# Optimization experiments

Hardware: AMD Instinct MI355X
Metric: run time of the kernel (lower is better)

The kernel has to match this reference:

```python
import jax, jax.numpy as jnp
import numpy as np

B, T, C = 2, 2048, 2048
H, KVH = 16, 4
HD = C // H            # head_dim = 128
REP = H // KVH         # q heads per kv head = 4


def _alibi_slopes(n_head):
    # get_slopes_power_of_2: start = 2^(-2^-(log2(H)-3)); s_h = start * start^h
    start = 2.0 ** (-(2.0 ** (-(np.log2(n_head) - 3.0))))
    return jnp.asarray([start ** (i + 1) for i in range(n_head)], jnp.float32)


def setup_inputs() -> dict:
    key = jax.random.key(0)
    ks = jax.random.split(key, 4)
    sc = 0.02
    return {
        "x": jax.random.normal(ks[0], (B, T, C), jnp.float32),
        "Wq": jax.random.normal(ks[1], (C, C), jnp.float32) * sc,
        "Wkv": jax.random.normal(ks[2], (C, HD * KVH * 2), jnp.float32) * sc,
        "Wo": jax.random.normal(ks[3], (C, C), jnp.float32) * sc,
        "bo": jnp.zeros((C,), jnp.float32),
    }


def reference(x, Wq, Wkv, Wo, bo):
    Bv, Tv, Cv = x.shape
    # projections
    q = (x @ Wq).reshape(Bv, Tv, H, HD).transpose(0, 2, 1, 3)      # (B,H,T,hd)
    k, v = jnp.split(x @ Wkv, 2, axis=-1)
    k = k.reshape(Bv, Tv, KVH, HD).transpose(0, 2, 1, 3)           # (B,KVH,T,hd)
    v = v.reshape(Bv, Tv, KVH, HD).transpose(0, 2, 1, 3)
    # torch .repeat tiles kv heads: query head h = r*KVH + g uses kv head g.
    qg = q.reshape(Bv, REP, KVH, Tv, HD)
    scores = jnp.einsum('brgtd,bgsd->brgts', qg, k) / jnp.sqrt(jnp.float32(HD))
    # ALiBi bias: tril((j - i) * slope_h), zero on/above diagonal region handled by causal mask
    idx = jnp.arange(Tv)
    diff = (idx[None, :] - idx[:, None]).astype(jnp.float32)       # j - i (negative below diag)
    slopes = _alibi_slopes(H).reshape(REP, KVH)                    # head h = r*KVH+g
    bias = jnp.tril(diff)[None, None] * slopes[:, :, None, None]   # (REP,KVH,T,T)
    causal = idx[None, :] <= idx[:, None]                          # (T,T)
    scores = jnp.where(causal[None, None, None], scores + bias[None], -jnp.inf)
    attn = jax.nn.softmax(scores, axis=-1)
    out = jnp.einsum('brgts,bgsd->brgtd', attn, v)                 # (B,REP,KVH,T,hd)
    out = out.reshape(Bv, H, Tv, HD).transpose(0, 2, 1, 3).reshape(Bv, Tv, Cv)
    return out @ Wo + bo
```

## Files before the change

kernel.cpp:

```cpp
#include <hip/hip_runtime.h>

typedef __attribute__((ext_vector_type(8))) __bf16 bf16x8;
typedef __attribute__((ext_vector_type(4))) float f32x4;

#define NEG_BIG (-1e30f)

__device__ __forceinline__ unsigned short f2b(float f) {
    unsigned int u = __float_as_uint(f);
    u += 0x7FFFu + ((u >> 16) & 1u);
    return (unsigned short)(u >> 16);
}
__device__ __forceinline__ unsigned cvtpk(float lo, float hi) {
    unsigned r;
    asm("v_cvt_pk_bf16_f32 %0, %1, %2" : "=v"(r) : "v"(lo), "v"(hi));
    return r;
}

typedef const __attribute__((address_space(1))) unsigned int* gas_ptr;
typedef __attribute__((address_space(3))) unsigned int* las_ptr;
__device__ __forceinline__ void gload16(const void* g, void* l) {
    __builtin_amdgcn_global_load_lds((gas_ptr)g, (las_ptr)l, 16, 0, 0);
}

__global__ __launch_bounds__(256) void k_convert(
    const float* __restrict__ x, unsigned short* __restrict__ xb, int n4)
{
    int i = blockIdx.x * 256 + threadIdx.x;
    if (i >= n4) return;
    float4 v = reinterpret_cast<const float4*>(x)[i];
    ushort4 h;
    h.x = f2b(v.x); h.y = f2b(v.y); h.z = f2b(v.z); h.w = f2b(v.w);
    reinterpret_cast<ushort4*>(xb)[i] = h;
}

__global__ __launch_bounds__(256) void k_transpose_all(
    const float* __restrict__ Wq, const float* __restrict__ Wkv,
    const float* __restrict__ Wo, unsigned short* __restrict__ Th, int K)
{
    __shared__ float tile[64][65];
    const int n0g = blockIdx.x * 64, k0 = blockIdx.y * 64;
    const float* W; int N, nloc;
    if (n0g < 2048)      { W = Wq;  N = 2048; nloc = n0g; }
    else if (n0g < 3072) { W = Wkv; N = 1024; nloc = n0g - 2048; }
    else                 { W = Wo;  N = 2048; nloc = n0g - 3072; }
    const int c = threadIdx.x & 63, r0 = threadIdx.x >> 6;
    for (int rr = r0; rr < 64; rr += 4)
        tile[rr][c] = W[(size_t)(k0 + rr) * N + nloc + c];
    __syncthreads();
    for (int rr = r0; rr < 64; rr += 4)
        Th[(size_t)(n0g + rr) * K + k0 + c] = f2b(tile[c][rr]);
}

__global__ __launch_bounds__(256) void k_gemm(
    const unsigned short* __restrict__ A, const unsigned short* __restrict__ B,
    void* __restrict__ CoutA, int NA, void* __restrict__ CoutB, int NB, int N1,
    const float* __restrict__ bias, int M, int K, int outF32)
{
    __shared__ __align__(16) unsigned short As[128][64];
    __shared__ __align__(16) unsigned short Bs[128][64];

    const int tid  = threadIdx.x;
    const int lane = tid & 63, wid = tid >> 6;
    const int wr = wid >> 1, wc = wid & 1;
    const int lrow = lane & 15, lko = (lane >> 4) << 3;
    const int bm = blockIdx.y, bn = blockIdx.x;

    const int srow = tid >> 3;
    const int scol = ((tid & 7) ^ (srow & 7)) << 3;
    const int wbase = wid * 1024;

    const int sw = (lrow & 7) << 3;
    const int c0 = lko ^ sw;
    const int c1 = (32 + lko) ^ sw;

    f32x4 acc[4][4] = {};

    const size_t aoff = (size_t)(bm * 128 + srow) * K + scol;
    const size_t boff = (size_t)(bn * 128 + srow) * K + scol;
    const size_t slab = (size_t)32 * K;

    for (int k0 = 0; k0 < K; k0 += 64) {
        #pragma unroll
        for (int s = 0; s < 4; ++s) {
            gload16(&A[aoff + s * slab + k0], (char*)&As[0][0] + s * 4096 + wbase);
            gload16(&B[boff + s * slab + k0], (char*)&Bs[0][0] + s * 4096 + wbase);
        }
        __syncthreads();

        #pragma unroll
        for (int kk2 = 0; kk2 < 2; ++kk2) {
            const int cc = kk2 ? c1 : c0;
            bf16x8 af[4], bf[4];
            #pragma unroll
            for (int m = 0; m < 4; ++m)
                af[m] = *reinterpret_cast<const bf16x8*>(&As[wr * 64 + m * 16 + lrow][cc]);
            #pragma unroll
            for (int n = 0; n < 4; ++n)
                bf[n] = *reinterpret_cast<const bf16x8*>(&Bs[wc * 64 + n * 16 + lrow][cc]);
            #pragma unroll
            for (int m = 0; m < 4; ++m)
                #pragma unroll
                for (int n = 0; n < 4; ++n)
                    acc[m][n] = __builtin_amdgcn_mfma_f32_16x16x32_bf16(af[m], bf[n], acc[m][n], 0, 0, 0);
        }
        __syncthreads();
    }

    const int rbase = bm * 128 + wr * 64 + ((lane >> 4) << 2);
    const int cbase = bn * 128 + wc * 64 + lrow;
    #pragma unroll
    for (int m = 0; m < 4; ++m)
        #pragma unroll
        for (int n = 0; n < 4; ++n) {
            const int col = cbase + n * 16;
            const float bv = bias ? bias[col] : 0.0f;
            const bool inA = (col < N1);
            const int ccol = inA ? col : (col - N1);
            const int cstr = inA ? NA : NB;
            void* base = inA ? CoutA : CoutB;
            #pragma unroll
            for (int r = 0; r < 4; ++r) {
                const size_t idx = (size_t)(rbase + m * 16 + r) * cstr + ccol;
                const float v = acc[m][n][r] + bv;
                if (outF32) ((float*)base)[idx] = v;
                else        ((unsigned short*)base)[idx] = f2b(v);
            }
        }
}

__global__ __launch_bounds__(512, 4) void k_attn(
    const unsigned short* __restrict__ Qb,
    const unsigned short* __restrict__ KVb,
    unsigned short* __restrict__ AO)
{
    __shared__ __align__(16) unsigned short Ksl[64][128];
    __shared__ __align__(16) unsigned short Vt[128][72];
    __shared__ __align__(16) unsigned short Psl[8][16][72];

    const int blk = blockIdx.x;
    const int idx = blk >> 3;
    const int sub = blk & 7;
    const int b   = sub >> 2;
    const int g   = sub & 3;
    const int chunk = (idx < 32) ? (63 - idx) : (idx - 32);
    const int q0  = chunk * 32;

    const int tid = threadIdx.x;
    const int lane = tid & 63;
    const int w = tid >> 6;
    const int h = (w & 3) * 4 + g;
    const int q0w = q0 + (w >> 2) * 16;
    const float slope = exp2f(-0.5f * (float)(h + 1));
    const float isq = 0.088388347648318447f;
    const int lrow = lane & 15;
    const int lko  = (lane >> 4) << 3;
    const int rowg = (lane >> 4) << 2;
    const int skey = tid >> 4;
    const int sd0  = (tid & 15) << 3;
    const int vdim = tid & 127;
    const int vkg  = tid >> 7;

    uint4 kreg[2];
    unsigned short vv[2][8];

    auto ldK = [&](int kb) {
        const int j0 = kb << 6;
        #pragma unroll
        for (int pp = 0; pp < 2; ++pp) {
            const int key = skey + pp * 32;
            kreg[pp] = *reinterpret_cast<const uint4*>(
                &KVb[(size_t)(b * 2048 + j0 + key) * 1024 + g * 128 + sd0]);
        }
    };
    auto wrK = [&]() {
        #pragma unroll
        for (int pp = 0; pp < 2; ++pp) {
            const int key = skey + pp * 32;
            *reinterpret_cast<uint4*>(&Ksl[key][sd0 ^ ((key & 7) << 3)]) = kreg[pp];
        }
    };
    auto ldV = [&](int kb) {
        const int j0 = kb << 6;
        #pragma unroll
        for (int gi = 0; gi < 2; ++gi) {
            const int kgi = gi * 4 + vkg;
            const size_t base = (size_t)(b * 2048 + j0 + kgi * 8) * 1024 + 512 + g * 128 + vdim;
            #pragma unroll
            for (int j = 0; j < 8; ++j)
                vv[gi][j] = KVb[base + (size_t)j * 1024];
        }
    };
    auto wrV = [&]() {
        #pragma unroll
        for (int gi = 0; gi < 2; ++gi) {
            const int kgi = gi * 4 + vkg;
            *reinterpret_cast<uint4*>(&Vt[vdim][kgi * 8]) =
                *reinterpret_cast<const uint4*>(&vv[gi][0]);
        }
    };

    bf16x8 qf[4];
    {
        const size_t qoff = (size_t)(b * 2048 + q0w + lrow) * 2048 + h * 128 + lko;
        #pragma unroll
        for (int kk = 0; kk < 4; ++kk)
            qf[kk] = *reinterpret_cast<const bf16x8*>(&Qb[qoff + kk * 32]);
    }

    f32x4 oacc[8] = {};
    float mrow = NEG_BIG, lsum = 0.f;
    const int nkb = (q0 + 32 + 63) >> 6;
    const int q = q0w + lrow;

    ldK(0); ldV(0);
    wrK(); wrV();
    __syncthreads();

    for (int kb = 0; kb < nkb; ++kb) {
        const int j0 = kb << 6;
        const bool pre = (kb + 1 < nkb);
        if (pre) { ldK(kb + 1); ldV(kb + 1); }

        f32x4 sa[4] = {};
        #pragma unroll
        for (int c = 0; c < 4; ++c) {
            const int krow = c * 16 + lrow;
            #pragma unroll
            for (int kk = 0; kk < 4; ++kk) {
                bf16x8 kf = *reinterpret_cast<const bf16x8*>(
                    &Ksl[krow][(kk * 32 + lko) ^ ((krow & 7) << 3)]);
                sa[c] = __builtin_amdgcn_mfma_f32_16x16x32_bf16(kf, qf[kk], sa[c], 0, 0, 0);
            }
        }

        float pv[4][4];
        float mt = NEG_BIG;
        #pragma unroll
        for (int c = 0; c < 4; ++c)
            #pragma unroll
            for (int r = 0; r < 4; ++r) {
                const int j = j0 + c * 16 + rowg + r;
                const float vsc = (j <= q) ? (sa[c][r] * isq + slope * (float)(j - q)) : NEG_BIG;
                pv[c][r] = vsc;
                mt = fmaxf(mt, vsc);
            }
        mt = fmaxf(mt, __shfl_xor(mt, 16));
        mt = fmaxf(mt, __shfl_xor(mt, 32));
        const float mn = fmaxf(mrow, mt);
        const float alpha = __expf(mrow - mn);
        mrow = mn;
        float s = 0.f;
        #pragma unroll
        for (int c = 0; c < 4; ++c)
            #pragma unroll
            for (int r = 0; r < 4; ++r) {
                const float pe = __expf(pv[c][r] - mn);
                pv[c][r] = pe;
                s += pe;
            }
        s += __shfl_xor(s, 16);
        s += __shfl_xor(s, 32);
        lsum = lsum * alpha + s;

        float ar[4];
        #pragma unroll
        for (int r = 0; r < 4; ++r) ar[r] = __shfl(alpha, rowg + r);
        #pragma unroll
        for (int f = 0; f < 8; ++f)
            #pragma unroll
            for (int r = 0; r < 4; ++r)
                oacc[f][r] *= ar[r];

        #pragma unroll
        for (int c = 0; c < 4; ++c) {
            uint2 pw;
            pw.x = cvtpk(pv[c][0], pv[c][1]);
            pw.y = cvtpk(pv[c][2], pv[c][3]);
            *reinterpret_cast<uint2*>(&Psl[w][lrow][c * 16 + rowg]) = pw;
        }
        asm volatile("s_waitcnt lgkmcnt(0)" ::: "memory");

        #pragma unroll
        for (int kk2 = 0; kk2 < 2; ++kk2) {
            bf16x8 pf = *reinterpret_cast<const bf16x8*>(&Psl[w][lrow][kk2 * 32 + lko]);
            #pragma unroll
            for (int nb = 0; nb < 8; ++nb) {
                bf16x8 vf = *reinterpret_cast<const bf16x8*>(&Vt[nb * 16 + lrow][kk2 * 32 + lko]);
                oacc[nb] = __builtin_amdgcn_mfma_f32_16x16x32_bf16(pf, vf, oacc[nb], 0, 0, 0);
            }
        }

        __syncthreads();
        if (pre) { wrK(); wrV(); }
        __syncthreads();
    }

    float lr[4];
    #pragma unroll
    for (int r = 0; r < 4; ++r) lr[r] = __shfl(lsum, rowg + r);
    #pragma unroll
    for (int nb = 0; nb < 8; ++nb)
        #pragma unroll
        for (int r = 0; r < 4; ++r) {
            const int row = q0w + rowg + r;
            const int col = h * 128 + nb * 16 + lrow;
            const float vo = oacc[nb][r] / lr[r];
            AO[(size_t)(b * 2048 + row) * 2048 + col] = f2b(vo);
        }
}

extern "C" void kernel_launch(void* const* d_in, const int* in_sizes, int n_in,
                              void* d_out, int out_size, void* d_ws, size_t ws_size,
                              hipStream_t stream)
{
    const float* x   = (const float*)d_in[0];
    const float* Wq  = (const float*)d_in[1];
    const float* Wkv = (const float*)d_in[2];
    const float* Wo  = (const float*)d_in[3];
    const float* bo  = (const float*)d_in[4];

    char* ws = (char*)d_ws;
    unsigned short* xb  = (unsigned short*)(ws + (size_t)0);
    unsigned short* Wt  = (unsigned short*)(ws + ((size_t)16 << 20));
    unsigned short* Qb  = (unsigned short*)(ws + ((size_t)36 << 20));
    unsigned short* KVb = (unsigned short*)(ws + ((size_t)52 << 20));

    k_convert<<<8192, 256, 0, stream>>>(x, xb, (2 * 2048 * 2048) / 4);

    k_transpose_all<<<dim3(80, 32), 256, 0, stream>>>(Wq, Wkv, Wo, Wt, 2048);

    k_gemm<<<dim3(24, 32), 256, 0, stream>>>(xb, Wt, Qb, 2048, KVb, 1024, 2048,
                                             nullptr, 4096, 2048, 0);

    k_attn<<<512, 512, 0, stream>>>(Qb, KVb, xb);

    k_gemm<<<dim3(16, 32), 256, 0, stream>>>(xb, Wt + (size_t)3072 * 2048, d_out, 2048,
                                             nullptr, 2048, 2048, bo, 4096, 2048, 1);
}
```

Before: 241.8 us.

## Merge prep kernels and double-buffer K tiles via direct global-to-LDS loads

Fuses the x conversion and weight transpose into one launch, which saves one kernel launch and its tail. In attention, K tiles are now loaded with global_load_lds straight into a double-buffered shared array, using a pre-swizzled source address. This removes the register staging and the explicit LDS write for K. It costs an extra 16KB of LDS, which may lower occupancy at 4 blocks per CU, and it relies on the async load finishing before the barrier.

```diff
diff --git a/kernel.cpp b/kernel.cpp
--- a/kernel.cpp
+++ b/kernel.cpp
@@ -22,23 +22,23 @@
     __builtin_amdgcn_global_load_lds((gas_ptr)g, (las_ptr)l, 16, 0, 0);
 }
 
-__global__ __launch_bounds__(256) void k_convert(
-    const float* __restrict__ x, unsigned short* __restrict__ xb, int n4)
-{
-    int i = blockIdx.x * 256 + threadIdx.x;
-    if (i >= n4) return;
-    float4 v = reinterpret_cast<const float4*>(x)[i];
-    ushort4 h;
-    h.x = f2b(v.x); h.y = f2b(v.y); h.z = f2b(v.z); h.w = f2b(v.w);
-    reinterpret_cast<ushort4*>(xb)[i] = h;
-}
-
-__global__ __launch_bounds__(256) void k_transpose_all(
+__global__ __launch_bounds__(256) void k_prep(
+    const float* __restrict__ x, unsigned short* __restrict__ xb,
     const float* __restrict__ Wq, const float* __restrict__ Wkv,
-    const float* __restrict__ Wo, unsigned short* __restrict__ Th, int K)
+    const float* __restrict__ Wo, unsigned short* __restrict__ Th)
 {
     __shared__ float tile[64][65];
-    const int n0g = blockIdx.x * 64, k0 = blockIdx.y * 64;
+    const int blk = blockIdx.x;
+    if (blk < 8192) {
+        const int i = blk * 256 + threadIdx.x;
+        float4 v = reinterpret_cast<const float4*>(x)[i];
+        ushort4 h;
+        h.x = f2b(v.x); h.y = f2b(v.y); h.z = f2b(v.z); h.w = f2b(v.w);
+        reinterpret_cast<ushort4*>(xb)[i] = h;
+        return;
+    }
+    const int bx = blk - 8192;
+    const int n0g = (bx % 80) * 64, k0 = (bx / 80) * 64;
     const float* W; int N, nloc;
     if (n0g < 2048)      { W = Wq;  N = 2048; nloc = n0g; }
     else if (n0g < 3072) { W = Wkv; N = 1024; nloc = n0g - 2048; }
@@ -48,7 +48,7 @@
         tile[rr][c] = W[(size_t)(k0 + rr) * N + nloc + c];
     __syncthreads();
     for (int rr = r0; rr < 64; rr += 4)
-        Th[(size_t)(n0g + rr) * K + k0 + c] = f2b(tile[c][rr]);
+        Th[(size_t)(n0g + rr) * 2048 + k0 + c] = f2b(tile[c][rr]);
 }
 
 __global__ __launch_bounds__(256) void k_gemm(
@@ -133,7 +133,7 @@
     const unsigned short* __restrict__ KVb,
     unsigned short* __restrict__ AO)
 {
-    __shared__ __align__(16) unsigned short Ksl[64][128];
+    __shared__ __align__(16) unsigned short Ksl[2][64][128];
     __shared__ __align__(16) unsigned short Vt[128][72];
     __shared__ __align__(16) unsigned short Psl[8][16][72];
 
@@ -157,26 +157,19 @@
     const int rowg = (lane >> 4) << 2;
     const int skey = tid >> 4;
     const int sd0  = (tid & 15) << 3;
+    const int ksrc = sd0 ^ ((skey & 7) << 3);
     const int vdim = tid & 127;
     const int vkg  = tid >> 7;
 
-    uint4 kreg[2];
     unsigned short vv[2][8];
 
-    auto ldK = [&](int kb) {
+    auto gloadK = [&](int kb, int buf) {
         const int j0 = kb << 6;
         #pragma unroll
         for (int pp = 0; pp < 2; ++pp) {
             const int key = skey + pp * 32;
-            kreg[pp] = *reinterpret_cast<const uint4*>(
-                &KVb[(size_t)(b * 2048 + j0 + key) * 1024 + g * 128 + sd0]);
-        }
-    };
-    auto wrK = [&]() {
-        #pragma unroll
-        for (int pp = 0; pp < 2; ++pp) {
-            const int key = skey + pp * 32;
-            *reinterpret_cast<uint4*>(&Ksl[key][sd0 ^ ((key & 7) << 3)]) = kreg[pp];
+            gload16(&KVb[(size_t)(b * 2048 + j0 + key) * 1024 + g * 128 + ksrc],
+                    (char*)&Ksl[buf][0][0] + pp * 8192 + tid * 16);
         }
     };
     auto ldV = [&](int kb) {
@@ -212,14 +205,16 @@
     const int nkb = (q0 + 32 + 63) >> 6;
     const int q = q0w + lrow;
 
-    ldK(0); ldV(0);
-    wrK(); wrV();
+    gloadK(0, 0);
+    ldV(0);
+    wrV();
     __syncthreads();
 
+    int cur = 0;
     for (int kb = 0; kb < nkb; ++kb) {
         const int j0 = kb << 6;
         const bool pre = (kb + 1 < nkb);
-        if (pre) { ldK(kb + 1); ldV(kb + 1); }
+        if (pre) { gloadK(kb + 1, cur ^ 1); ldV(kb + 1); }
 
         f32x4 sa[4] = {};
         #pragma unroll
@@ -228,7 +223,7 @@
             #pragma unroll
             for (int kk = 0; kk < 4; ++kk) {
                 bf16x8 kf = *reinterpret_cast<const bf16x8*>(
-                    &Ksl[krow][(kk * 32 + lko) ^ ((krow & 7) << 3)]);
+                    &Ksl[cur][krow][(kk * 32 + lko) ^ ((krow & 7) << 3)]);
                 sa[c] = __builtin_amdgcn_mfma_f32_16x16x32_bf16(kf, qf[kk], sa[c], 0, 0, 0);
             }
         }
@@ -291,8 +286,9 @@
         }
 
         __syncthreads();
-        if (pre) { wrK(); wrV(); }
+        if (pre) wrV();
         __syncthreads();
+        cur ^= 1;
     }
 
     float lr[4];
@@ -325,9 +321,7 @@
     unsigned short* Qb  = (unsigned short*)(ws + ((size_t)36 << 20));
     unsigned short* KVb = (unsigned short*)(ws + ((size_t)52 << 20));
 
-    k_convert<<<8192, 256, 0, stream>>>(x, xb, (2 * 2048 * 2048) / 4);
-
-    k_transpose_all<<<dim3(80, 32), 256, 0, stream>>>(Wq, Wkv, Wo, Wt, 2048);
+    k_prep<<<10752, 256, 0, stream>>>(x, xb, Wq, Wkv, Wo, Wt);
 
     k_gemm<<<dim3(24, 32), 256, 0, stream>>>(xb, Wt, Qb, 2048, KVb, 1024, 2048,
                                              nullptr, 4096, 2048, 0);
```

After: 221.8 us (median of 2 runs). -8.2%, faster.
